# Optimization experiments

Hardware: AMD Instinct MI355X
Metric: run time of the kernel (lower is better)

The kernel has to match this reference:

```python
import jax, jax.numpy as jnp
import numpy as np

D_MODEL = 1024
NHEAD = 16
HEAD_DIM = D_MODEL // NHEAD
MAX_SEQ = 512


def _rope_tables(seq_len):
    dim_half = HEAD_DIM // 2
    pos = jnp.arange(seq_len, dtype=jnp.float32)
    freqs = 1.0 / (10000.0 ** (jnp.arange(dim_half, dtype=jnp.float32) / dim_half))
    angles = pos[:, None] * freqs[None, :]  # [S, dim_half]
    return jnp.sin(angles), jnp.cos(angles)


def setup_inputs() -> dict:
    key = jax.random.key(0)
    ks = jax.random.split(key, 5)
    x = jax.random.normal(ks[0], (8, 512, D_MODEL), dtype=jnp.float32)
    s = 1.0 / np.sqrt(D_MODEL)
    W_qkv = jax.random.uniform(ks[1], (D_MODEL, 3 * D_MODEL), jnp.float32, -s, s)
    b_qkv = jax.random.uniform(ks[2], (3 * D_MODEL,), jnp.float32, -s, s)
    W_out = jax.random.uniform(ks[3], (D_MODEL, D_MODEL), jnp.float32, -s, s)
    b_out = jax.random.uniform(ks[4], (D_MODEL,), jnp.float32, -s, s)
    return {"x": x, "W_qkv": W_qkv, "b_qkv": b_qkv, "W_out": W_out, "b_out": b_out}


def reference(x, W_qkv, b_qkv, W_out, b_out):
    B, S, _ = x.shape
    qkv = x @ W_qkv + b_qkv                                   # [B,S,3D]
    qkv = qkv.reshape(B, S, 3, NHEAD, HEAD_DIM).transpose(2, 0, 3, 1, 4)
    q, k, v = qkv[0], qkv[1], qkv[2]                          # [B,H,S,Dh]
    sin, cos = _rope_tables(S)                                # [S, Dh/2]
    dh = HEAD_DIM // 2
    q1, q2 = q[..., :dh], q[..., dh:]
    k1, k2 = k[..., :dh], k[..., dh:]
    q = jnp.concatenate([q1 * cos - q2 * sin, q1 * sin + q2 * cos], axis=-1)
    k = jnp.concatenate([k1 * cos - k2 * sin, k1 * sin + k2 * cos], axis=-1)
    scores = jnp.einsum('bhqd,bhkd->bhqk', q, k) / np.sqrt(HEAD_DIM)
    attn = jax.nn.softmax(scores, axis=-1)                    # dropout: eval mode (identity)
    out = jnp.einsum('bhqk,bhkd->bhqd', attn, v)
    out = out.transpose(0, 2, 1, 3).reshape(B, S, D_MODEL)
    return out @ W_out + b_out
```

## Files before the change

kernel.cpp:

```cpp
#include <hip/hip_runtime.h>
#include <hip/hip_bf16.h>

#define NB 8
#define SEQ 512
#define DMODEL 1024
#define NHEAD 16
#define HDIM 64
typedef __hip_bfloat16 bf16;
typedef __attribute__((ext_vector_type(8))) short short8;
typedef __attribute__((ext_vector_type(4))) float f32x4;

__device__ __forceinline__ void glds16(const void* g, void* l) {
    __builtin_amdgcn_global_load_lds(
        (const __attribute__((address_space(1))) unsigned int*)g,
        (__attribute__((address_space(3))) unsigned int*)l, 16, 0, 0);
}

__global__ __launch_bounds__(256)
void cast_bf16_k(const float* __restrict__ X, bf16* __restrict__ Xb) {
    int i = (blockIdx.x * 256 + threadIdx.x) * 8;
    float4 v0 = *(const float4*)&X[i];
    float4 v1 = *(const float4*)&X[i + 4];
    bf16 o[8];
    o[0] = __float2bfloat16(v0.x); o[1] = __float2bfloat16(v0.y);
    o[2] = __float2bfloat16(v0.z); o[3] = __float2bfloat16(v0.w);
    o[4] = __float2bfloat16(v1.x); o[5] = __float2bfloat16(v1.y);
    o[6] = __float2bfloat16(v1.z); o[7] = __float2bfloat16(v1.w);
    *(uint4*)&Xb[i] = *(uint4*)o;
}

__global__ __launch_bounds__(256)
void transpose_cast_k(const float* __restrict__ W, bf16* __restrict__ Wt,
                      int R, int C) {
    __shared__ float t[64][65];
    int k0 = blockIdx.y * 64, n0 = blockIdx.x * 64;
    int c = threadIdx.x & 63, r = threadIdx.x >> 6;
    #pragma unroll 4
    for (int i = 0; i < 16; ++i)
        t[r + i * 4][c] = W[(size_t)(k0 + r + i * 4) * C + n0 + c];
    __syncthreads();
    #pragma unroll 4
    for (int i = 0; i < 16; ++i)
        Wt[(size_t)(n0 + r + i * 4) * R + k0 + c] = __float2bfloat16(t[c][r + i * 4]);
}

#define GEMM_MAINLOOP_SB(Agp, Bgp, Asm_, Bsm_)                                \
    int tid = threadIdx.x;                                                    \
    int lane = tid & 63, wid = tid >> 6;                                      \
    int wr = wid >> 1, wc = wid & 1;                                          \
    int lj = lane & 15, li = lane >> 4;                                       \
    int srow = lane >> 3, ssl = lane & 7;                                     \
    f32x4 acc[4][4] = {};                                                     \
    for (int ks = 0; ks < 16; ++ks) {                                         \
        int k0 = ks * 64;                                                     \
        _Pragma("unroll")                                                     \
        for (int q = 0; q < 4; ++q) {                                         \
            int seg = wid * 4 + q;                                            \
            int row = seg * 8 + srow;                                         \
            int cg = ssl ^ (row & 7);                                         \
            glds16(Agp + ((size_t)(m0 + row) * 1024 + k0 + cg * 8),           \
                   (char*)(Asm_) + seg * 1024);                               \
            glds16(Bgp + ((size_t)(n0 + row) * 1024 + k0 + cg * 8),           \
                   (char*)(Bsm_) + seg * 1024);                               \
        }                                                                     \
        __syncthreads();                                                      \
        _Pragma("unroll")                                                     \
        for (int kk = 0; kk < 2; ++kk) {                                      \
            short8 af[4], bfr[4];                                             \
            _Pragma("unroll")                                                 \
            for (int mf = 0; mf < 4; ++mf) {                                  \
                int r = wr * 64 + mf * 16 + lj;                               \
                int ck = kk * 4 + li;                                         \
                af[mf] = *(const short8*)((const char*)(Asm_) +               \
                          (r * 128 + ((ck ^ (r & 7)) * 16)));                 \
            }                                                                 \
            _Pragma("unroll")                                                 \
            for (int nf = 0; nf < 4; ++nf) {                                  \
                int r = wc * 64 + nf * 16 + lj;                               \
                int ck = kk * 4 + li;                                         \
                bfr[nf] = *(const short8*)((const char*)(Bsm_) +              \
                          (r * 128 + ((ck ^ (r & 7)) * 16)));                 \
            }                                                                 \
            _Pragma("unroll")                                                 \
            for (int mf = 0; mf < 4; ++mf)                                    \
                _Pragma("unroll")                                             \
                for (int nf = 0; nf < 4; ++nf)                                \
                    acc[mf][nf] = __builtin_amdgcn_mfma_f32_16x16x32_bf16(    \
                        af[mf], bfr[nf], acc[mf][nf], 0, 0, 0);               \
        }                                                                     \
        __syncthreads();                                                      \
    }

__global__ __launch_bounds__(256)
void qkv_mfma_k(const bf16* __restrict__ Xb, const bf16* __restrict__ Wt,
                const float* __restrict__ bias,
                bf16* __restrict__ Qb, bf16* __restrict__ Kb, bf16* __restrict__ Vt) {
    __shared__ __align__(16) short SM[16640];
    short* Asm = SM;
    short* Bsm = SM + 8192;
    int m0 = blockIdx.y * 128, n0 = blockIdx.x * 128;
    GEMM_MAINLOOP_SB(Xb, Wt, Asm, Bsm)
    int c = n0 >> 10;
    if (c == 2) {
        short (*Vl)[130] = (short(*)[130])SM;
        #pragma unroll
        for (int nf = 0; nf < 4; ++nf) {
            int cl = wc * 64 + nf * 16 + lj;
            float bv = bias[n0 + cl];
            #pragma unroll
            for (int mf = 0; mf < 4; ++mf)
                #pragma unroll
                for (int j = 0; j < 4; ++j) {
                    int ml = wr * 64 + mf * 16 + li * 4 + j;
                    *(bf16*)&Vl[cl][ml] = __float2bfloat16(acc[mf][nf][j] + bv);
                }
        }
        __syncthreads();
        int bb = m0 >> 9, s0 = m0 & 511;
        int hbase = (n0 & 1023) >> 6;
        #pragma unroll
        for (int it = 0; it < 8; ++it) {
            int cl = it * 16 + wid * 4 + li;
            int off = lj * 8;
            uint4 v = *(const uint4*)&Vl[cl][off];
            int hsub = cl >> 6, p = cl & 63;
            size_t dst = ((size_t)(bb * NHEAD + hbase + hsub) * HDIM + p) * SEQ
                         + s0 + off;
            *(uint4*)&Vt[dst] = v;
        }
    } else {
        int ncol = n0 + wc * 64;
        int h = (ncol & 1023) >> 6;
        bf16* dst = (c == 0) ? Qb : Kb;
        #pragma unroll
        for (int nf = 0; nf < 2; ++nf) {
            int p = nf * 16 + lj;
            float b1 = bias[ncol + p], b2 = bias[ncol + p + 32];
            float freq = __expf(-(float)p * 0.28782313662425574f);
            #pragma unroll
            for (int mf = 0; mf < 4; ++mf) {
                #pragma unroll
                for (int j = 0; j < 4; ++j) {
                    int m = m0 + wr * 64 + mf * 16 + li * 4 + j;
                    int bb = m >> 9, s = m & 511;
                    float v1 = acc[mf][nf][j] + b1;
                    float v2 = acc[mf][nf + 2][j] + b2;
                    float sv, cv;
                    __sincosf((float)s * freq, &sv, &cv);
                    float o1 = v1 * cv - v2 * sv;
                    float o2 = v1 * sv + v2 * cv;
                    size_t base = ((size_t)(bb * NHEAD + h) * SEQ + s) * HDIM;
                    dst[base + p]      = __float2bfloat16(o1);
                    dst[base + p + 32] = __float2bfloat16(o2);
                }
            }
        }
    }
}

__global__ __launch_bounds__(256)
void out_mfma_k(const bf16* __restrict__ Ab, const bf16* __restrict__ Wt,
                const float* __restrict__ bias, float* __restrict__ out) {
    __shared__ __align__(16) short SM[16384];
    short* Asm = SM;
    short* Bsm = SM + 8192;
    int m0 = blockIdx.y * 128, n0 = blockIdx.x * 128;
    GEMM_MAINLOOP_SB(Ab, Wt, Asm, Bsm)
    int col0 = n0 + wc * 64;
    #pragma unroll
    for (int nf = 0; nf < 4; ++nf) {
        int col = col0 + nf * 16 + lj;
        float bv = bias[col];
        #pragma unroll
        for (int mf = 0; mf < 4; ++mf)
            #pragma unroll
            for (int j = 0; j < 4; ++j) {
                int m = m0 + wr * 64 + mf * 16 + li * 4 + j;
                out[(size_t)m * DMODEL + col] = acc[mf][nf][j] + bv;
            }
    }
}

__global__ __launch_bounds__(256)
void attn_mfma_k(const bf16* __restrict__ Qb, const bf16* __restrict__ Kb,
                 const bf16* __restrict__ Vt, bf16* __restrict__ Ab) {
    __shared__ __align__(16) short Qsm[64 * 64];
    __shared__ __align__(16) short Ksm[64 * 64];
    __shared__ __align__(16) short Vsm[64 * 64];
    __shared__ __align__(16) short Psm[64 * 64];
    int tid = threadIdx.x;
    int lane = tid & 63, wid = tid >> 6;
    int lj = lane & 15, li = lane >> 4;
    int bh = blockIdx.x >> 3, qt = blockIdx.x & 7;
    const bf16* Qp = Qb + ((size_t)bh * SEQ + qt * 64) * HDIM;
    const bf16* Kp = Kb + (size_t)bh * SEQ * HDIM;
    const bf16* Vp = Vt + (size_t)bh * HDIM * SEQ;
    int srow = lane >> 3, ssl = lane & 7;
    #pragma unroll
    for (int q = 0; q < 2; ++q) {
        int seg = wid * 2 + q;
        int row = seg * 8 + srow;
        int cg = ssl ^ (row & 7);
        glds16(Qp + ((size_t)row * 64 + cg * 8), (char*)Qsm + seg * 1024);
    }
    float m_[4], l_[4];
    f32x4 acc_o[4] = {};
    #pragma unroll
    for (int j = 0; j < 4; ++j) { m_[j] = -1e30f; l_[j] = 0.f; }
    __syncthreads();
    for (int kt = 0; kt < 8; ++kt) {
        #pragma unroll
        for (int q = 0; q < 2; ++q) {
            int seg = wid * 2 + q;
            int row = seg * 8 + srow;
            int cg = ssl ^ (row & 7);
            glds16(Kp + ((size_t)(kt * 64 + row) * 64 + cg * 8),
                   (char*)Ksm + seg * 1024);
            glds16(Vp + ((size_t)row * SEQ + kt * 64 + cg * 8),
                   (char*)Vsm + seg * 1024);
        }
        __syncthreads();
        f32x4 sacc[4] = {};
        #pragma unroll
        for (int kk = 0; kk < 2; ++kk) {
            int r = wid * 16 + lj;
            int ck = kk * 4 + li;
            short8 af = *(const short8*)((const char*)Qsm +
                         (r * 128 + ((ck ^ (r & 7)) * 16)));
            #pragma unroll
            for (int nf = 0; nf < 4; ++nf) {
                int rb = nf * 16 + lj;
                short8 kf = *(const short8*)((const char*)Ksm +
                             (rb * 128 + ((ck ^ (rb & 7)) * 16)));
                sacc[nf] = __builtin_amdgcn_mfma_f32_16x16x32_bf16(af, kf, sacc[nf], 0, 0, 0);
            }
        }
        float p[4][4];
        #pragma unroll
        for (int j = 0; j < 4; ++j) {
            float s0 = sacc[0][j] * 0.125f, s1 = sacc[1][j] * 0.125f;
            float s2 = sacc[2][j] * 0.125f, s3 = sacc[3][j] * 0.125f;
            float tm = fmaxf(fmaxf(s0, s1), fmaxf(s2, s3));
            tm = fmaxf(tm, __shfl_xor(tm, 1));
            tm = fmaxf(tm, __shfl_xor(tm, 2));
            tm = fmaxf(tm, __shfl_xor(tm, 4));
            tm = fmaxf(tm, __shfl_xor(tm, 8));
            float mn = fmaxf(m_[j], tm);
            float sc = __expf(m_[j] - mn);
            p[0][j] = __expf(s0 - mn); p[1][j] = __expf(s1 - mn);
            p[2][j] = __expf(s2 - mn); p[3][j] = __expf(s3 - mn);
            float ts = p[0][j] + p[1][j] + p[2][j] + p[3][j];
            ts += __shfl_xor(ts, 1); ts += __shfl_xor(ts, 2);
            ts += __shfl_xor(ts, 4); ts += __shfl_xor(ts, 8);
            l_[j] = l_[j] * sc + ts;
            m_[j] = mn;
            acc_o[0][j] *= sc; acc_o[1][j] *= sc;
            acc_o[2][j] *= sc; acc_o[3][j] *= sc;
        }
        #pragma unroll
        for (int nf = 0; nf < 4; ++nf)
            #pragma unroll
            for (int j = 0; j < 4; ++j) {
                int row = wid * 16 + li * 4 + j;
                int col = nf * 16 + lj;
                int cl = col >> 3;
                *(bf16*)((char*)Psm + row * 128 + ((cl ^ (row & 7)) * 16) +
                         (col & 7) * 2) = __float2bfloat16(p[nf][j]);
            }
        #pragma unroll
        for (int kk = 0; kk < 2; ++kk) {
            int r = wid * 16 + lj;
            int ck = kk * 4 + li;
            short8 pa = *(const short8*)((const char*)Psm +
                         (r * 128 + ((ck ^ (r & 7)) * 16)));
            #pragma unroll
            for (int nf = 0; nf < 4; ++nf) {
                int rb = nf * 16 + lj;
                short8 vf = *(const short8*)((const char*)Vsm +
                             (rb * 128 + ((ck ^ (rb & 7)) * 16)));
                acc_o[nf] = __builtin_amdgcn_mfma_f32_16x16x32_bf16(pa, vf, acc_o[nf], 0, 0, 0);
            }
        }
        __syncthreads();
    }
    int b = bh >> 4, h = bh & 15;
    #pragma unroll
    for (int j = 0; j < 4; ++j) {
        float inv = 1.0f / l_[j];
        int s = qt * 64 + wid * 16 + li * 4 + j;
        #pragma unroll
        for (int nf = 0; nf < 4; ++nf) {
            int d = nf * 16 + lj;
            Ab[((size_t)b * SEQ + s) * DMODEL + h * 64 + d] =
                __float2bfloat16(acc_o[nf][j] * inv);
        }
    }
}

extern "C" void kernel_launch(void* const* d_in, const int* in_sizes, int n_in,
                              void* d_out, int out_size, void* d_ws, size_t ws_size,
                              hipStream_t stream) {
    const float *x = nullptr, *Wqkv = nullptr, *bqkv = nullptr,
                *Wout = nullptr, *bout = nullptr;
    for (int i = 0; i < n_in; ++i) {
        switch (in_sizes[i]) {
            case NB * SEQ * DMODEL:   x    = (const float*)d_in[i]; break;
            case DMODEL * 3 * DMODEL: Wqkv = (const float*)d_in[i]; break;
            case 3 * DMODEL:          bqkv = (const float*)d_in[i]; break;
            case DMODEL * DMODEL:     Wout = (const float*)d_in[i]; break;
            case DMODEL:              bout = (const float*)d_in[i]; break;
        }
    }
    if (!x)    x    = (const float*)d_in[0];
    if (!Wqkv) Wqkv = (const float*)d_in[1];
    if (!bqkv) bqkv = (const float*)d_in[2];
    if (!Wout) Wout = (const float*)d_in[3];
    if (!bout) bout = (const float*)d_in[4];
    float* out = (float*)d_out;

    char* ws = (char*)d_ws;
    bf16* Xb     = (bf16*)(ws);
    bf16* Ab     = (bf16*)(ws);
    bf16* Wqkv_t = (bf16*)(ws + 8388608);
    bf16* Wout_t = (bf16*)(ws + 14680064);
    bf16* Qb     = (bf16*)(ws + 16777216);
    bf16* Kb     = (bf16*)(ws + 25165824);
    bf16* Vt     = (bf16*)(ws + 33554432);

    cast_bf16_k<<<2048, 256, 0, stream>>>(x, Xb);
    transpose_cast_k<<<dim3(48, 16), 256, 0, stream>>>(Wqkv, Wqkv_t, DMODEL, 3 * DMODEL);
    transpose_cast_k<<<dim3(16, 16), 256, 0, stream>>>(Wout, Wout_t, DMODEL, DMODEL);
    qkv_mfma_k<<<dim3(24, 32), 256, 0, stream>>>(Xb, Wqkv_t, bqkv, Qb, Kb, Vt);
    attn_mfma_k<<<NB * NHEAD * 8, 256, 0, stream>>>(Qb, Kb, Vt, Ab);
    out_mfma_k<<<dim3(8, 32), 256, 0, stream>>>(Ab, Wout_t, bout, out);
}
```

Before: 186.5 us.

## Double-buffer LDS tiles in GEMM mainloop and use incremental RoPE rotation

```diff
diff --git a/kernel.cpp b/kernel.cpp
--- a/kernel.cpp
+++ b/kernel.cpp
@@ -44,26 +44,45 @@
         Wt[(size_t)(n0 + r + i * 4) * R + k0 + c] = __float2bfloat16(t[c][r + i * 4]);
 }
 
-#define GEMM_MAINLOOP_SB(Agp, Bgp, Asm_, Bsm_)                                \
+#define GEMM_MAINLOOP_PIPE(Agp, Bgp, Asm_, Bsm_)                              \
     int tid = threadIdx.x;                                                    \
     int lane = tid & 63, wid = tid >> 6;                                      \
     int wr = wid >> 1, wc = wid & 1;                                          \
     int lj = lane & 15, li = lane >> 4;                                       \
     int srow = lane >> 3, ssl = lane & 7;                                     \
     f32x4 acc[4][4] = {};                                                     \
+    _Pragma("unroll")                                                         \
+    for (int q = 0; q < 4; ++q) {                                             \
+        int seg = wid * 4 + q;                                                \
+        int row = seg * 8 + srow;                                             \
+        int cg = ssl ^ (row & 7);                                             \
+        glds16(Agp + ((size_t)(m0 + row) * 1024 + cg * 8),                    \
+               (char*)(Asm_) + seg * 1024);                                   \
+        glds16(Bgp + ((size_t)(n0 + row) * 1024 + cg * 8),                    \
+               (char*)(Bsm_) + seg * 1024);                                   \
+    }                                                                         \
     for (int ks = 0; ks < 16; ++ks) {                                         \
-        int k0 = ks * 64;                                                     \
-        _Pragma("unroll")                                                     \
-        for (int q = 0; q < 4; ++q) {                                         \
-            int seg = wid * 4 + q;                                            \
-            int row = seg * 8 + srow;                                         \
-            int cg = ssl ^ (row & 7);                                         \
-            glds16(Agp + ((size_t)(m0 + row) * 1024 + k0 + cg * 8),           \
-                   (char*)(Asm_) + seg * 1024);                               \
-            glds16(Bgp + ((size_t)(n0 + row) * 1024 + k0 + cg * 8),           \
-                   (char*)(Bsm_) + seg * 1024);                               \
+        int cur = ks & 1;                                                     \
+        if (ks + 1 < 16) {                                                    \
+            int k0 = (ks + 1) * 64;                                           \
+            _Pragma("unroll")                                                 \
+            for (int q = 0; q < 4; ++q) {                                     \
+                int seg = wid * 4 + q;                                        \
+                int row = seg * 8 + srow;                                     \
+                int cg = ssl ^ (row & 7);                                     \
+                glds16(Agp + ((size_t)(m0 + row) * 1024 + k0 + cg * 8),       \
+                       (char*)(Asm_) + (cur ^ 1) * 16384 + seg * 1024);       \
+                glds16(Bgp + ((size_t)(n0 + row) * 1024 + k0 + cg * 8),       \
+                       (char*)(Bsm_) + (cur ^ 1) * 16384 + seg * 1024);       \
+            }                                                                 \
+            asm volatile("s_waitcnt vmcnt(8)" ::: "memory");                  \
+        } else {                                                              \
+            asm volatile("s_waitcnt vmcnt(0)" ::: "memory");                  \
         }                                                                     \
-        __syncthreads();                                                      \
+        __builtin_amdgcn_s_barrier();                                         \
+        asm volatile("" ::: "memory");                                        \
+        const char* Abuf_ = (const char*)(Asm_) + cur * 16384;                \
+        const char* Bbuf_ = (const char*)(Bsm_) + cur * 16384;                \
         _Pragma("unroll")                                                     \
         for (int kk = 0; kk < 2; ++kk) {                                      \
             short8 af[4], bfr[4];                                             \
@@ -71,14 +90,14 @@
             for (int mf = 0; mf < 4; ++mf) {                                  \
                 int r = wr * 64 + mf * 16 + lj;                               \
                 int ck = kk * 4 + li;                                         \
-                af[mf] = *(const short8*)((const char*)(Asm_) +               \
+                af[mf] = *(const short8*)(Abuf_ +                             \
                           (r * 128 + ((ck ^ (r & 7)) * 16)));                 \
             }                                                                 \
             _Pragma("unroll")                                                 \
             for (int nf = 0; nf < 4; ++nf) {                                  \
                 int r = wc * 64 + nf * 16 + lj;                               \
                 int ck = kk * 4 + li;                                         \
-                bfr[nf] = *(const short8*)((const char*)(Bsm_) +              \
+                bfr[nf] = *(const short8*)(Bbuf_ +                            \
                           (r * 128 + ((ck ^ (r & 7)) * 16)));                 \
             }                                                                 \
             _Pragma("unroll")                                                 \
@@ -88,18 +107,20 @@
                     acc[mf][nf] = __builtin_amdgcn_mfma_f32_16x16x32_bf16(    \
                         af[mf], bfr[nf], acc[mf][nf], 0, 0, 0);               \
         }                                                                     \
-        __syncthreads();                                                      \
+        asm volatile("s_waitcnt lgkmcnt(0)" ::: "memory");                    \
+        __builtin_amdgcn_s_barrier();                                         \
+        asm volatile("" ::: "memory");                                        \
     }
 
 __global__ __launch_bounds__(256)
 void qkv_mfma_k(const bf16* __restrict__ Xb, const bf16* __restrict__ Wt,
                 const float* __restrict__ bias,
                 bf16* __restrict__ Qb, bf16* __restrict__ Kb, bf16* __restrict__ Vt) {
-    __shared__ __align__(16) short SM[16640];
+    __shared__ __align__(16) short SM[32768];
     short* Asm = SM;
-    short* Bsm = SM + 8192;
+    short* Bsm = SM + 16384;
     int m0 = blockIdx.y * 128, n0 = blockIdx.x * 128;
-    GEMM_MAINLOOP_SB(Xb, Wt, Asm, Bsm)
+    GEMM_MAINLOOP_PIPE(Xb, Wt, Asm, Bsm)
     int c = n0 >> 10;
     if (c == 2) {
         short (*Vl)[130] = (short(*)[130])SM;
@@ -137,21 +158,26 @@
             int p = nf * 16 + lj;
             float b1 = bias[ncol + p], b2 = bias[ncol + p + 32];
             float freq = __expf(-(float)p * 0.28782313662425574f);
+            float sf, cf;
+            __sincosf(freq, &sf, &cf);
             #pragma unroll
             for (int mf = 0; mf < 4; ++mf) {
+                int mb = m0 + wr * 64 + mf * 16 + li * 4;
+                int bb = mb >> 9, s0 = mb & 511;
+                float sv, cv;
+                __sincosf((float)s0 * freq, &sv, &cv);
                 #pragma unroll
                 for (int j = 0; j < 4; ++j) {
-                    int m = m0 + wr * 64 + mf * 16 + li * 4 + j;
-                    int bb = m >> 9, s = m & 511;
                     float v1 = acc[mf][nf][j] + b1;
                     float v2 = acc[mf][nf + 2][j] + b2;
-                    float sv, cv;
-                    __sincosf((float)s * freq, &sv, &cv);
                     float o1 = v1 * cv - v2 * sv;
                     float o2 = v1 * sv + v2 * cv;
-                    size_t base = ((size_t)(bb * NHEAD + h) * SEQ + s) * HDIM;
+                    size_t base = ((size_t)(bb * NHEAD + h) * SEQ + s0 + j) * HDIM;
                     dst[base + p]      = __float2bfloat16(o1);
                     dst[base + p + 32] = __float2bfloat16(o2);
+                    float cn = cv * cf - sv * sf;
+                    sv = sv * cf + cv * sf;
+                    cv = cn;
                 }
             }
         }
@@ -161,11 +187,11 @@
 __global__ __launch_bounds__(256)
 void out_mfma_k(const bf16* __restrict__ Ab, const bf16* __restrict__ Wt,
                 const float* __restrict__ bias, float* __restrict__ out) {
-    __shared__ __align__(16) short SM[16384];
+    __shared__ __align__(16) short SM[32768];
     short* Asm = SM;
-    short* Bsm = SM + 8192;
+    short* Bsm = SM + 16384;
     int m0 = blockIdx.y * 128, n0 = blockIdx.x * 128;
-    GEMM_MAINLOOP_SB(Ab, Wt, Asm, Bsm)
+    GEMM_MAINLOOP_PIPE(Ab, Wt, Asm, Bsm)
     int col0 = n0 + wc * 64;
     #pragma unroll
     for (int nf = 0; nf < 4; ++nf) {
```

Result: faster. 170.6 us (-8.5%).
